# Performance work log

Hardware: AMD Instinct MI355X
Metric: run time of the kernel (lower is better)

The kernel has to match this reference:

```python
import math
import jax, jax.numpy as jnp
import numpy as np

DIM = 1024
NUM_HEADS = 16
HEAD_DIM = DIM // NUM_HEADS


def rotate_half(x):
    x1, x2 = jnp.split(x, 2, axis=-1)
    return jnp.concatenate((-x2, x1), axis=-1)


def rope_cos_sin(seq_len, head_dim, dtype):
    # angles: (S, D/2); duplicated to (S, D) so it applies to full head_dim
    pos = jnp.arange(seq_len, dtype=dtype)[:, None]
    inv = jnp.exp(jnp.arange(0, head_dim, 2, dtype=dtype) * (-(math.log(10000.0) / head_dim)))
    angles = pos * inv[None, :]
    angles = jnp.concatenate((angles, angles), axis=-1)  # (S, D)
    return jnp.cos(angles), jnp.sin(angles)


def setup_inputs() -> dict:
    key = jax.random.key(0)
    ks = jax.random.split(key, 5)
    B, S, C = 8, 1024, DIM
    scale = 1.0 / math.sqrt(C)
    return {
        "x": jax.random.normal(ks[0], (B, S, C), dtype=jnp.float32),
        "W_qkv": jax.random.normal(ks[1], (C, 3 * C), dtype=jnp.float32) * scale,
        "b_qkv": jax.random.normal(ks[2], (3 * C,), dtype=jnp.float32) * 0.02,
        "W_proj": jax.random.normal(ks[3], (C, C), dtype=jnp.float32) * scale,
        "b_proj": jax.random.normal(ks[4], (C,), dtype=jnp.float32) * 0.02,
    }


def reference(x, W_qkv, b_qkv, W_proj, b_proj):
    B, S, C = x.shape
    H, D = NUM_HEADS, C // NUM_HEADS
    scale = D ** -0.5

    qkv = x @ W_qkv + b_qkv                       # (B, S, 3C)
    qkv = qkv.reshape(B, S, 3, H, D).transpose(2, 0, 3, 1, 4)  # (3, B, H, S, D)
    q, k, v = qkv[0], qkv[1], qkv[2]

    cos, sin = rope_cos_sin(S, D, x.dtype)        # (S, D) each, broadcast over B,H
    q = q * cos + rotate_half(q) * sin
    k = k * cos + rotate_half(k) * sin

    attn = jnp.einsum("bhqd,bhkd->bhqk", q, k) * scale
    attn = jax.nn.softmax(attn, axis=-1)
    out = jnp.einsum("bhqk,bhkd->bhqd", attn, v)  # (B, H, S, D)
    out = out.transpose(0, 2, 1, 3).reshape(B, S, C)
    return out @ W_proj + b_proj
```

## Files before the change

### kernel.cpp

```cpp
#include <hip/hip_runtime.h>
#include <hip/hip_fp16.h>
#include <math.h>


typedef _Float16 half_t;
typedef _Float16 half8 __attribute__((ext_vector_type(8)));
typedef _Float16 half4v __attribute__((ext_vector_type(4)));
typedef float f32x4 __attribute__((ext_vector_type(4)));
typedef float f32x16 __attribute__((ext_vector_type(16)));

#define MFMA16(a, b, c) __builtin_amdgcn_mfma_f32_16x16x32_f16(a, b, c, 0, 0, 0)
#define MFMA32(a, b, c) __builtin_amdgcn_mfma_f32_32x32x16_f16(a, b, c, 0, 0, 0)

__device__ __forceinline__ void gload_lds16(const half_t* g, half_t* lds) {
  __builtin_amdgcn_global_load_lds(
      (const __attribute__((address_space(1))) void*)g,
      (__attribute__((address_space(3))) void*)lds, 16, 0, 0);
}

__device__ __forceinline__ void prep_transpose(const float* __restrict__ in,
                                               half_t* __restrict__ out,
                                               int rows, int cols, int bx,
                                               int by, half_t (*tile)[33]) {
  int c0 = bx * 32, r0 = by * 32;
  int tx = threadIdx.x & 31, g = threadIdx.x >> 5;
#pragma unroll
  for (int i = 0; i < 4; i++) {
    int r = g * 4 + i;
    tile[r][tx] = (half_t)in[(size_t)(r0 + r) * cols + c0 + tx];
  }
  __syncthreads();
#pragma unroll
  for (int i = 0; i < 4; i++) {
    int cc = g * 4 + i;
    out[(size_t)(c0 + cc) * rows + r0 + tx] = tile[tx][cc];
  }
}

__global__ __launch_bounds__(256) void k_prep(
    const float* __restrict__ x, half_t* __restrict__ x16,
    const float* __restrict__ Wqkv, half_t* __restrict__ WqkvT,
    const float* __restrict__ Wproj, half_t* __restrict__ WprojT,
    float2* __restrict__ rope) {
  __shared__ half_t tile[32][33];
  int bid = blockIdx.x;
  if (bid < 8192) {
    int i = bid * 256 + threadIdx.x;
    float4 v = ((const float4*)x)[i];
    half4v h;
    h.x = (half_t)v.x; h.y = (half_t)v.y; h.z = (half_t)v.z; h.w = (half_t)v.w;
    ((half4v*)x16)[i] = h;
  } else if (bid < 11264) {
    int idx = bid - 8192;
    prep_transpose(Wqkv, WqkvT, 1024, 3072, idx % 96, idx / 96, tile);
  } else if (bid < 12288) {
    int idx = bid - 11264;
    prep_transpose(Wproj, WprojT, 1024, 1024, idx & 31, idx >> 5, tile);
  } else {
    int idx = (bid - 12288) * 256 + threadIdx.x;
    int s = idx >> 5, jj = idx & 31;
    float inv = expf(-0.28782313662425572f * (float)jj);
    float ang = (float)s * inv;
    float sn, cs;
    sincosf(ang, &sn, &cs);
    rope[idx] = make_float2(cs, sn);
  }
}

template <int MODE>
__global__ __launch_bounds__(256) void k_gemm(
    const half_t* __restrict__ A, const half_t* __restrict__ Bt,
    const float* __restrict__ bias, const float2* __restrict__ rope,
    half_t* __restrict__ Qo, half_t* __restrict__ Ko, half_t* __restrict__ Vo,
    float* __restrict__ Fo) {
  __shared__ alignas(16) half_t smem[17408];
  half_t* As = smem;
  half_t* Bs = smem + 8192;
  const int t = threadIdx.x;
  const int lane = t & 63, w = t >> 6;
  const int c32 = lane & 31, kh = lane >> 5;
  const int m0 = blockIdx.y * 128, n0 = blockIdx.x * 128;
  const int wm = (w >> 1) * 64, wn = (w & 1) * 64;

  f32x16 acc[2][2] = {};

  for (int kt = 0; kt < 1024; kt += 64) {
    __syncthreads();
#pragma unroll
    for (int cc = 0; cc < 4; cc++) {
      int lg = (w * 4 + cc) * 64 + lane;
      int row = lg >> 3;
      int gs = (lg & 7) ^ (row & 7);
      gload_lds16(A + (size_t)(m0 + row) * 1024 + kt + gs * 8,
                  As + (w * 4 + cc) * 512);
      gload_lds16(Bt + (size_t)(n0 + row) * 1024 + kt + gs * 8,
                  Bs + (w * 4 + cc) * 512);
    }
    __syncthreads();
#pragma unroll
    for (int ks = 0; ks < 4; ks++) {
      half8 af[2], bf[2];
#pragma unroll
      for (int i = 0; i < 2; i++) {
        int mr = wm + i * 32 + c32;
        af[i] = *(const half8*)(As + mr * 64 + (((ks * 2 + kh) ^ (mr & 7)) * 8));
        int nr = wn + i * 32 + c32;
        bf[i] = *(const half8*)(Bs + nr * 64 + (((ks * 2 + kh) ^ (nr & 7)) * 8));
      }
#pragma unroll
      for (int i = 0; i < 2; i++)
#pragma unroll
        for (int j = 0; j < 2; j++) acc[i][j] = MFMA32(af[i], bf[j], acc[i][j]);
    }
  }

  if (MODE == 0) {
    const int which = n0 >> 10;
    const int b = m0 >> 10, sbase = m0 & 1023;
    if (which == 2) {
      __syncthreads();
      half_t* T = smem;
#pragma unroll
      for (int i = 0; i < 2; i++)
#pragma unroll
        for (int j = 0; j < 2; j++) {
          int nl = wn + j * 32 + c32;
          float bs = bias[n0 + nl];
#pragma unroll
          for (int a = 0; a < 4; a++) {
            half4v pk;
#pragma unroll
            for (int q = 0; q < 4; q++)
              pk[q] = (half_t)(acc[i][j][a * 4 + q] + bs);
            *(half4v*)(T + nl * 136 + wm + i * 32 + kh * 4 + a * 8) = pk;
          }
        }
      __syncthreads();
#pragma unroll
      for (int u = 0; u < 8; u++) {
        int ci = u * 256 + t;
        int drow = ci >> 4, scol = (ci & 15) * 8;
        half8 val = *(const half8*)(T + drow * 136 + scol);
        int n = n0 + drow;
        int hh = (n >> 6) & 15, d = n & 63;
        *(half8*)(Vo + ((size_t)((b * 16 + hh) * 64 + d)) * 1024 + sbase + scol) = val;
      }
    } else {
      __syncthreads();
      half_t* T = smem;
      const float qsc = (which == 0) ? 0.125f : 1.0f;
#pragma unroll
      for (int i = 0; i < 2; i++)
#pragma unroll
        for (int a = 0; a < 4; a++)
#pragma unroll
          for (int q = 0; q < 4; q++) {
            int ml = wm + i * 32 + a * 8 + kh * 4 + q;
            int s = sbase + ml;
            float2 tr = rope[(s << 5) | c32];
#pragma unroll
            for (int j = 0; j < 2; j++) {
              int nl = wn + j * 32 + c32;
              int n = n0 + nl;
              float v = acc[i][j][a * 4 + q] + bias[n];
              float pr = acc[i][j ^ 1][a * 4 + q] + bias[n ^ 32];
              float rv = (j == 0) ? (v * tr.x - pr * tr.y)
                                  : (v * tr.x + pr * tr.y);
              T[ml * 136 + nl] = (half_t)(rv * qsc);
            }
          }
      __syncthreads();
      half_t* dst = (which == 0) ? Qo : Ko;
#pragma unroll
      for (int u = 0; u < 8; u++) {
        int ci = u * 256 + t;
        int mrow = ci >> 4, ch = ci & 15;
        half8 val = *(const half8*)(T + mrow * 136 + ch * 8);
        int s = sbase + mrow;
        int n = n0 + ch * 8;
        int hh = (n >> 6) & 15, d = n & 63;
        *(half8*)(dst + ((size_t)((b * 16 + hh) * 1024 + s)) * 64 + d) = val;
      }
    }
  } else {
#pragma unroll
    for (int i = 0; i < 2; i++)
#pragma unroll
      for (int a = 0; a < 4; a++)
#pragma unroll
        for (int q = 0; q < 4; q++) {
          int gm = m0 + wm + i * 32 + a * 8 + kh * 4 + q;
#pragma unroll
          for (int j = 0; j < 2; j++) {
            int n = n0 + wn + j * 32 + c32;
            Fo[(size_t)gm * 1024 + n] = acc[i][j][a * 4 + q] + bias[n];
          }
        }
  }
}

__global__ __launch_bounds__(256) void k_attn(const half_t* __restrict__ Qg_,
                                              const half_t* __restrict__ Kg_,
                                              const half_t* __restrict__ Vg_,
                                              half_t* __restrict__ Og) {
  __shared__ alignas(16) half_t Qs[8192];
  __shared__ alignas(16) half_t Ks[4096];
  __shared__ alignas(16) half_t Vs[4096];
  __shared__ alignas(16) half_t Ps[128 * 72];
  __shared__ float ilbuf[128];
  const int t = threadIdx.x, lane = t & 63, w = t >> 6;
  const int quad = lane >> 4, cl = lane & 15;
  const int bh = blockIdx.x, q0 = blockIdx.y * 128;
  const half_t* Qg = Qg_ + (size_t)bh * 65536;
  const half_t* Kg = Kg_ + (size_t)bh * 65536;
  const half_t* Vg = Vg_ + (size_t)bh * 65536;

#pragma unroll
  for (int cc = 0; cc < 4; cc++) {
    int lg = (w * 4 + cc) * 64 + lane;
    int row = lg >> 3;
    int gs = (lg & 7) ^ (row & 7);
    gload_lds16(Qg + (size_t)(q0 + row) * 64 + gs * 8, Qs + (w * 4 + cc) * 512);
  }
  __syncthreads();

  half8 qf[2][2];
#pragma unroll
  for (int ks = 0; ks < 2; ks++)
#pragma unroll
    for (int j = 0; j < 2; j++) {
      int qr = w * 32 + j * 16 + cl;
      qf[ks][j] = *(const half8*)(Qs + qr * 64 + (((ks * 4 + quad) ^ (qr & 7)) * 8));
    }

  f32x4 oacc[2][4] = {};
  float lsum[2] = {0.f, 0.f};

  for (int kt = 0; kt < 1024; kt += 64) {
    __syncthreads();
#pragma unroll
    for (int cc = 0; cc < 2; cc++) {
      int lg = (w * 2 + cc) * 64 + lane;
      int row = lg >> 3;
      int gs = (lg & 7) ^ (row & 7);
      gload_lds16(Kg + (size_t)(kt + row) * 64 + gs * 8, Ks + (w * 2 + cc) * 512);
      gload_lds16(Vg + (size_t)row * 1024 + kt + gs * 8, Vs + (w * 2 + cc) * 512);
    }
    __syncthreads();

    f32x4 sacc[4][2] = {};
#pragma unroll
    for (int ks = 0; ks < 2; ks++) {
      half8 kf[4];
#pragma unroll
      for (int i = 0; i < 4; i++) {
        int kr = i * 16 + cl;
        kf[i] = *(const half8*)(Ks + kr * 64 + (((ks * 4 + quad) ^ (kr & 7)) * 8));
      }
#pragma unroll
      for (int i = 0; i < 4; i++)
#pragma unroll
        for (int j = 0; j < 2; j++)
          sacc[i][j] = MFMA16(kf[i], qf[ks][j], sacc[i][j]);
    }

#pragma unroll
    for (int i = 0; i < 4; i++)
#pragma unroll
      for (int j = 0; j < 2; j++) {
        float p0 = __expf(sacc[i][j][0] - 8.f);
        float p1 = __expf(sacc[i][j][1] - 8.f);
        float p2 = __expf(sacc[i][j][2] - 8.f);
        float p3 = __expf(sacc[i][j][3] - 8.f);
        lsum[j] += (p0 + p1) + (p2 + p3);
        half4v pk;
        pk.x = (half_t)p0; pk.y = (half_t)p1; pk.z = (half_t)p2; pk.w = (half_t)p3;
        *(half4v*)(Ps + (w * 32 + j * 16 + cl) * 72 + i * 16 + quad * 4) = pk;
      }

#pragma unroll
    for (int ks = 0; ks < 2; ks++) {
      half8 pf[2], vf[4];
#pragma unroll
      for (int i = 0; i < 2; i++)
        pf[i] = *(const half8*)(Ps + (w * 32 + i * 16 + cl) * 72 + ks * 32 + quad * 8);
#pragma unroll
      for (int j = 0; j < 4; j++) {
        int dr = j * 16 + cl;
        vf[j] = *(const half8*)(Vs + dr * 64 + (((ks * 4 + quad) ^ (dr & 7)) * 8));
      }
#pragma unroll
      for (int i = 0; i < 2; i++)
#pragma unroll
        for (int j = 0; j < 4; j++) oacc[i][j] = MFMA16(pf[i], vf[j], oacc[i][j]);
    }
  }

#pragma unroll
  for (int j = 0; j < 2; j++) {
    float l = lsum[j];
    l += __shfl_xor(l, 16);
    l += __shfl_xor(l, 32);
    if (quad == 0) ilbuf[w * 32 + j * 16 + cl] = 1.f / l;
  }

  const int b = bh >> 4, hh = bh & 15;
#pragma unroll
  for (int i = 0; i < 2; i++)
#pragma unroll
    for (int r = 0; r < 4; r++) {
      float sc = ilbuf[w * 32 + i * 16 + quad * 4 + r];
      int srow = q0 + w * 32 + i * 16 + quad * 4 + r;
#pragma unroll
      for (int j = 0; j < 4; j++) {
        int d = j * 16 + cl;
        Og[((size_t)(b * 1024 + srow)) * 1024 + hh * 64 + d] =
            (half_t)(oacc[i][j][r] * sc);
      }
    }
}

extern "C" void kernel_launch(void* const* d_in, const int* in_sizes, int n_in,
                              void* d_out, int out_size, void* d_ws,
                              size_t ws_size, hipStream_t stream) {
  (void)in_sizes; (void)n_in; (void)out_size; (void)ws_size;
  const float* x = (const float*)d_in[0];
  const float* Wqkv = (const float*)d_in[1];
  const float* bqkv = (const float*)d_in[2];
  const float* Wproj = (const float*)d_in[3];
  const float* bproj = (const float*)d_in[4];
  float* out = (float*)d_out;

  half_t* ws = (half_t*)d_ws;
  half_t* x16 = ws;
  half_t* WqkvT = ws + 8388608;
  half_t* WprojT = ws + 11534336;
  half_t* Q16 = ws + 12582912;
  half_t* K16 = ws + 20971520;
  half_t* V16 = ws + 29360128;
  float2* rope = (float2*)(ws + 37748736);
  half_t* O16 = x16;

  k_prep<<<12416, 256, 0, stream>>>(x, x16, Wqkv, WqkvT, Wproj, WprojT, rope);
  k_gemm<0><<<dim3(24, 64), 256, 0, stream>>>(x16, WqkvT, bqkv, rope, Q16, K16,
                                              V16, nullptr);
  k_attn<<<dim3(128, 8), 256, 0, stream>>>(Q16, K16, V16, O16);
  k_gemm<1><<<dim3(8, 64), 256, 0, stream>>>(O16, WprojT, bproj, nullptr,
                                             nullptr, nullptr, nullptr, out);
}
```

Baseline: 252.3 us.

## Enlarge GEMM block tile to 256x128 with 512 threads and two-pass epilogue

```diff
diff --git a/kernel.cpp b/kernel.cpp
--- a/kernel.cpp
+++ b/kernel.cpp
@@ -68,33 +68,47 @@
 }
 
 template <int MODE>
-__global__ __launch_bounds__(256) void k_gemm(
+__global__ __launch_bounds__(512, 4) void k_gemm(
     const half_t* __restrict__ A, const half_t* __restrict__ Bt,
     const float* __restrict__ bias, const float2* __restrict__ rope,
     half_t* __restrict__ Qo, half_t* __restrict__ Ko, half_t* __restrict__ Vo,
     float* __restrict__ Fo) {
-  __shared__ alignas(16) half_t smem[17408];
+  __shared__ alignas(16) half_t smem[24576];
   half_t* As = smem;
-  half_t* Bs = smem + 8192;
+  half_t* Bs = smem + 16384;
   const int t = threadIdx.x;
   const int lane = t & 63, w = t >> 6;
   const int c32 = lane & 31, kh = lane >> 5;
-  const int m0 = blockIdx.y * 128, n0 = blockIdx.x * 128;
-  const int wm = (w >> 1) * 64, wn = (w & 1) * 64;
+  const int wr = w >> 1, wc = w & 1;
+  const int wm = wr * 64, wn = wc * 64;
+  const int m0 = blockIdx.y * 256, n0 = blockIdx.x * 128;
 
   f32x16 acc[2][2] = {};
 
   for (int kt = 0; kt < 1024; kt += 64) {
     __syncthreads();
 #pragma unroll
-    for (int cc = 0; cc < 4; cc++) {
-      int lg = (w * 4 + cc) * 64 + lane;
-      int row = lg >> 3;
-      int gs = (lg & 7) ^ (row & 7);
+    for (int c = 0; c < 3; c++) {
+      int gid = c * 512 + t;
+      int row = gid >> 3;
+      int gs = (gid & 7) ^ (row & 7);
       gload_lds16(A + (size_t)(m0 + row) * 1024 + kt + gs * 8,
-                  As + (w * 4 + cc) * 512);
+                  As + c * 4096 + w * 512);
+    }
+    {
+      int gid = 3 * 512 + t;
+      int row = gid >> 3;
+      int gs = (gid & 7) ^ (row & 7);
+      gload_lds16(A + (size_t)(m0 + row) * 1024 + kt + gs * 8,
+                  As + 3 * 4096 + w * 512);
+    }
+#pragma unroll
+    for (int c = 0; c < 2; c++) {
+      int gid = c * 512 + t;
+      int row = gid >> 3;
+      int gs = (gid & 7) ^ (row & 7);
       gload_lds16(Bt + (size_t)(n0 + row) * 1024 + kt + gs * 8,
-                  Bs + (w * 4 + cc) * 512);
+                  Bs + c * 4096 + w * 512);
     }
     __syncthreads();
 #pragma unroll
@@ -120,66 +134,79 @@
     if (which == 2) {
       __syncthreads();
       half_t* T = smem;
-#pragma unroll
-      for (int i = 0; i < 2; i++)
-#pragma unroll
-        for (int j = 0; j < 2; j++) {
-          int nl = wn + j * 32 + c32;
-          float bs = bias[n0 + nl];
-#pragma unroll
-          for (int a = 0; a < 4; a++) {
-            half4v pk;
-#pragma unroll
-            for (int q = 0; q < 4; q++)
-              pk[q] = (half_t)(acc[i][j][a * 4 + q] + bs);
-            *(half4v*)(T + nl * 136 + wm + i * 32 + kh * 4 + a * 8) = pk;
-          }
-        }
-      __syncthreads();
-#pragma unroll
-      for (int u = 0; u < 8; u++) {
-        int ci = u * 256 + t;
-        int drow = ci >> 4, scol = (ci & 15) * 8;
-        half8 val = *(const half8*)(T + drow * 136 + scol);
-        int n = n0 + drow;
-        int hh = (n >> 6) & 15, d = n & 63;
-        *(half8*)(Vo + ((size_t)((b * 16 + hh) * 64 + d)) * 1024 + sbase + scol) = val;
+      for (int rm = 0; rm < 2; ++rm) {
+        if (rm) __syncthreads();
+        if ((wr >> 1) == rm) {
+          const int mbase = (wr & 1) * 64;
+#pragma unroll
+          for (int i = 0; i < 2; i++)
+#pragma unroll
+            for (int j = 0; j < 2; j++) {
+              int nl = wn + j * 32 + c32;
+              float bs = bias[n0 + nl];
+#pragma unroll
+              for (int a = 0; a < 4; a++) {
+                half4v pk;
+#pragma unroll
+                for (int q = 0; q < 4; q++)
+                  pk[q] = (half_t)(acc[i][j][a * 4 + q] + bs);
+                *(half4v*)(T + nl * 136 + mbase + i * 32 + kh * 4 + a * 8) = pk;
+              }
+            }
+        }
+        __syncthreads();
+#pragma unroll
+        for (int u = 0; u < 4; u++) {
+          int ci = u * 512 + t;
+          int drow = ci >> 4, scol = (ci & 15) * 8;
+          half8 val = *(const half8*)(T + drow * 136 + scol);
+          int n = n0 + drow;
+          int hh = (n >> 6) & 15, d = n & 63;
+          *(half8*)(Vo + ((size_t)((b * 16 + hh) * 64 + d)) * 1024 + sbase +
+                    rm * 128 + scol) = val;
+        }
       }
     } else {
       __syncthreads();
       half_t* T = smem;
       const float qsc = (which == 0) ? 0.125f : 1.0f;
-#pragma unroll
-      for (int i = 0; i < 2; i++)
-#pragma unroll
-        for (int a = 0; a < 4; a++)
-#pragma unroll
-          for (int q = 0; q < 4; q++) {
-            int ml = wm + i * 32 + a * 8 + kh * 4 + q;
-            int s = sbase + ml;
-            float2 tr = rope[(s << 5) | c32];
-#pragma unroll
-            for (int j = 0; j < 2; j++) {
-              int nl = wn + j * 32 + c32;
-              int n = n0 + nl;
-              float v = acc[i][j][a * 4 + q] + bias[n];
-              float pr = acc[i][j ^ 1][a * 4 + q] + bias[n ^ 32];
-              float rv = (j == 0) ? (v * tr.x - pr * tr.y)
-                                  : (v * tr.x + pr * tr.y);
-              T[ml * 136 + nl] = (half_t)(rv * qsc);
-            }
-          }
-      __syncthreads();
       half_t* dst = (which == 0) ? Qo : Ko;
-#pragma unroll
-      for (int u = 0; u < 8; u++) {
-        int ci = u * 256 + t;
-        int mrow = ci >> 4, ch = ci & 15;
-        half8 val = *(const half8*)(T + mrow * 136 + ch * 8);
-        int s = sbase + mrow;
-        int n = n0 + ch * 8;
-        int hh = (n >> 6) & 15, d = n & 63;
-        *(half8*)(dst + ((size_t)((b * 16 + hh) * 1024 + s)) * 64 + d) = val;
+      for (int rm = 0; rm < 2; ++rm) {
+        if (rm) __syncthreads();
+        if ((wr >> 1) == rm) {
+          const int mbase = (wr & 1) * 64;
+#pragma unroll
+          for (int i = 0; i < 2; i++)
+#pragma unroll
+            for (int a = 0; a < 4; a++)
+#pragma unroll
+              for (int q = 0; q < 4; q++) {
+                int mlr = mbase + i * 32 + a * 8 + kh * 4 + q;
+                int s = sbase + rm * 128 + mlr;
+                float2 tr = rope[(s << 5) | c32];
+#pragma unroll
+                for (int j = 0; j < 2; j++) {
+                  int nl = wn + j * 32 + c32;
+                  int n = n0 + nl;
+                  float v = acc[i][j][a * 4 + q] + bias[n];
+                  float pr = acc[i][j ^ 1][a * 4 + q] + bias[n ^ 32];
+                  float rv = (j == 0) ? (v * tr.x - pr * tr.y)
+                                      : (v * tr.x + pr * tr.y);
+                  T[mlr * 136 + nl] = (half_t)(rv * qsc);
+                }
+              }
+        }
+        __syncthreads();
+#pragma unroll
+        for (int u = 0; u < 4; u++) {
+          int ci = u * 512 + t;
+          int mrow = ci >> 4, ch = ci & 15;
+          half8 val = *(const half8*)(T + mrow * 136 + ch * 8);
+          int s = sbase + rm * 128 + mrow;
+          int n = n0 + ch * 8;
+          int hh = (n >> 6) & 15, d = n & 63;
+          *(half8*)(dst + ((size_t)((b * 16 + hh) * 1024 + s)) * 64 + d) = val;
+        }
       }
     }
   } else {
@@ -342,9 +369,9 @@
   half_t* O16 = x16;
 
   k_prep<<<12416, 256, 0, stream>>>(x, x16, Wqkv, WqkvT, Wproj, WprojT, rope);
-  k_gemm<0><<<dim3(24, 64), 256, 0, stream>>>(x16, WqkvT, bqkv, rope, Q16, K16,
+  k_gemm<0><<<dim3(24, 32), 512, 0, stream>>>(x16, WqkvT, bqkv, rope, Q16, K16,
                                               V16, nullptr);
   k_attn<<<dim3(128, 8), 256, 0, stream>>>(Q16, K16, V16, O16);
-  k_gemm<1><<<dim3(8, 64), 256, 0, stream>>>(O16, WprojT, bproj, nullptr,
+  k_gemm<1><<<dim3(8, 32), 512, 0, stream>>>(O16, WprojT, bproj, nullptr,
                                              nullptr, nullptr, nullptr, out);
 }
```

New measurement: 312.2 us. 1.24x slower.

## Double-buffer GEMM LDS tiles to overlap global loads with MFMA compute

Applied to the files above, without the earlier changes.

```diff
diff --git a/kernel.cpp b/kernel.cpp
--- a/kernel.cpp
+++ b/kernel.cpp
@@ -67,15 +67,28 @@
   }
 }
 
+#define GEMM_STAGE(KT, DB)                                                   \
+  {                                                                          \
+    half_t* As_ = (DB);                                                      \
+    half_t* Bs_ = (DB) + 8192;                                               \
+    _Pragma("unroll") for (int cc_ = 0; cc_ < 4; cc_++) {                    \
+      int lg_ = (w * 4 + cc_) * 64 + lane;                                   \
+      int row_ = lg_ >> 3;                                                   \
+      int gs_ = (lg_ & 7) ^ (row_ & 7);                                      \
+      gload_lds16(A + (size_t)(m0 + row_) * 1024 + (KT) + gs_ * 8,           \
+                  As_ + (w * 4 + cc_) * 512);                                \
+      gload_lds16(Bt + (size_t)(n0 + row_) * 1024 + (KT) + gs_ * 8,          \
+                  Bs_ + (w * 4 + cc_) * 512);                                \
+    }                                                                        \
+  }
+
 template <int MODE>
 __global__ __launch_bounds__(256) void k_gemm(
     const half_t* __restrict__ A, const half_t* __restrict__ Bt,
     const float* __restrict__ bias, const float2* __restrict__ rope,
     half_t* __restrict__ Qo, half_t* __restrict__ Ko, half_t* __restrict__ Vo,
     float* __restrict__ Fo) {
-  __shared__ alignas(16) half_t smem[17408];
-  half_t* As = smem;
-  half_t* Bs = smem + 8192;
+  __shared__ alignas(16) half_t smem[32768];
   const int t = threadIdx.x;
   const int lane = t & 63, w = t >> 6;
   const int c32 = lane & 31, kh = lane >> 5;
@@ -84,19 +97,20 @@
 
   f32x16 acc[2][2] = {};
 
-  for (int kt = 0; kt < 1024; kt += 64) {
-    __syncthreads();
-#pragma unroll
-    for (int cc = 0; cc < 4; cc++) {
-      int lg = (w * 4 + cc) * 64 + lane;
-      int row = lg >> 3;
-      int gs = (lg & 7) ^ (row & 7);
-      gload_lds16(A + (size_t)(m0 + row) * 1024 + kt + gs * 8,
-                  As + (w * 4 + cc) * 512);
-      gload_lds16(Bt + (size_t)(n0 + row) * 1024 + kt + gs * 8,
-                  Bs + (w * 4 + cc) * 512);
-    }
-    __syncthreads();
+  GEMM_STAGE(0, smem);
+
+  for (int tt = 0; tt < 16; ++tt) {
+    half_t* As = smem + (tt & 1) * 16384;
+    half_t* Bs = As + 8192;
+    if (tt < 15) {
+      GEMM_STAGE((tt + 1) * 64, smem + ((tt + 1) & 1) * 16384);
+      asm volatile("s_waitcnt vmcnt(8)" ::: "memory");
+    } else {
+      asm volatile("s_waitcnt vmcnt(0)" ::: "memory");
+    }
+    __builtin_amdgcn_sched_barrier(0);
+    __builtin_amdgcn_s_barrier();
+    __builtin_amdgcn_sched_barrier(0);
 #pragma unroll
     for (int ks = 0; ks < 4; ks++) {
       half8 af[2], bf[2];
@@ -112,6 +126,8 @@
 #pragma unroll
         for (int j = 0; j < 2; j++) acc[i][j] = MFMA32(af[i], bf[j], acc[i][j]);
     }
+    __builtin_amdgcn_sched_barrier(0);
+    __builtin_amdgcn_s_barrier();
   }
 
   if (MODE == 0) {
```

Measured after the change: 266.3 us. 1.06x slower.
